# Kernel tuning notes

Measured on AMD Instinct MI355X. Metric: run time of the kernel, lower is better.

The kernel has to match this reference:

```python
import jax, jax.numpy as jnp
import numpy as np

D_MODEL = 256
D_STATE = 128          # d_model // 2
D_CONV = 4
EXPAND = 4
D_INNER = EXPAND * D_MODEL  # 1024
DT_RANK = (D_MODEL + 15) // 16  # 16
N_HEADS = 8
D_FF = 4 * D_MODEL
EPS = 1e-6


def layer_norm(x, a, b):
    # torch LayerNorm-like but with unbiased std (ddof=1) per the source
    mean = jnp.mean(x, axis=-1, keepdims=True)
    d = x.shape[-1]
    var = jnp.sum((x - mean) ** 2, axis=-1, keepdims=True) / (d - 1)
    std = jnp.sqrt(var)
    return a * (x - mean) / (std + EPS) + b


def silu(x):
    return x * jax.nn.sigmoid(x)


def mamba(x, in_proj_w, conv_w, conv_b, x_proj_w, dt_proj_w, dt_proj_b, A_log, Dp, out_proj_w):
    B, L, _ = x.shape
    xz = jnp.einsum('bld,ed->ble', x, in_proj_w)  # (B,L,2*D_INNER)
    xi, z = xz[..., :D_INNER], xz[..., D_INNER:]
    # causal depthwise conv1d over L
    xp = jnp.pad(xi, ((0, 0), (D_CONV - 1, 0), (0, 0)))
    u = conv_b
    for k in range(D_CONV):
        u = u + xp[:, k:k + L, :] * conv_w[:, k]
    u = silu(u)  # (B,L,D_INNER)
    dbl = jnp.einsum('bld,ed->ble', u, x_proj_w)  # (B,L,DT_RANK+2*D_STATE)
    dt = dbl[..., :DT_RANK]
    Bm = dbl[..., DT_RANK:DT_RANK + D_STATE]
    Cm = dbl[..., DT_RANK + D_STATE:]
    dt = jax.nn.softplus(jnp.einsum('blr,dr->bld', dt, dt_proj_w) + dt_proj_b)  # (B,L,D_INNER)
    A = -jnp.exp(A_log)  # (D_INNER, D_STATE)
    dA = jnp.exp(jnp.einsum('bld,dn->bldn', dt, A))          # (B,L,Din,N)
    dBu = jnp.einsum('bld,bln,bld->bldn', dt, Bm, u)          # (B,L,Din,N)

    def step(h, inp):
        dA_t, dBu_t, C_t = inp
        h = dA_t * h + dBu_t                    # (B,Din,N)
        y = jnp.einsum('bdn,bn->bd', h, C_t)    # (B,Din)
        return h, y

    h0 = jnp.zeros((B, D_INNER, D_STATE), dtype=x.dtype)
    _, ys = jax.lax.scan(step, h0, (jnp.swapaxes(dA, 0, 1), jnp.swapaxes(dBu, 0, 1), jnp.swapaxes(Cm, 0, 1)))
    y = jnp.swapaxes(ys, 0, 1) + u * Dp  # (B,L,Din)
    y = y * silu(z)
    return jnp.einsum('ble,de->bld', y, out_proj_w)


def cross_attention(q_in, kv_in, mask, wq_w, wq_b, wk_w, wk_b, wv_w, wv_b, wo_w, wo_b):
    B, Lq, _ = q_in.shape
    Lk = kv_in.shape[1]
    dk = D_MODEL // N_HEADS
    q = (jnp.einsum('bld,ed->ble', q_in, wq_w) + wq_b).reshape(B, Lq, N_HEADS, dk).transpose(0, 2, 1, 3)
    k = (jnp.einsum('bld,ed->ble', kv_in, wk_w) + wk_b).reshape(B, Lk, N_HEADS, dk).transpose(0, 2, 1, 3)
    v = (jnp.einsum('bld,ed->ble', kv_in, wv_w) + wv_b).reshape(B, Lk, N_HEADS, dk).transpose(0, 2, 1, 3)
    scores = jnp.einsum('bhqd,bhkd->bhqk', q, k) / np.sqrt(dk)
    # mask: (B,1,Lk) bool -> broadcast (B,1,1,Lk)
    scores = jnp.where(mask[:, None, :, :], scores, jnp.finfo(scores.dtype).min)
    p = jax.nn.softmax(scores, axis=-1)
    o = jnp.einsum('bhqk,bhkd->bhqd', p, v).transpose(0, 2, 1, 3).reshape(B, Lq, D_MODEL)
    return jnp.einsum('ble,de->bld', o, wo_w) + wo_b


def setup_inputs() -> dict:
    key = jax.random.key(0)
    ks = jax.random.split(key, 24)
    s = 0.02
    B, L, Lm = 2, 512, 512
    inp = {
        'x': jax.random.normal(ks[0], (B, L, D_MODEL), jnp.float32),
        'memory': jax.random.normal(ks[1], (B, Lm, D_MODEL), jnp.float32),
        'src_mask': jnp.ones((B, 1, Lm), bool),
        'tgt_mask': jnp.ones((B, 1, L), bool),
        # mamba params
        'in_proj_w': jax.random.normal(ks[2], (2 * D_INNER, D_MODEL)) * s,
        'conv_w': jax.random.normal(ks[3], (D_INNER, D_CONV)) * s,
        'conv_b': jnp.zeros((D_INNER,)),
        'x_proj_w': jax.random.normal(ks[4], (DT_RANK + 2 * D_STATE, D_INNER)) * s,
        'dt_proj_w': jax.random.normal(ks[5], (D_INNER, DT_RANK)) * s,
        'dt_proj_b': jnp.log(jnp.expm1(0.01)) * jnp.ones((D_INNER,)),
        'A_log': jnp.log(jnp.broadcast_to(jnp.arange(1, D_STATE + 1, dtype=jnp.float32), (D_INNER, D_STATE))),
        'Dp': jnp.ones((D_INNER,)),
        'out_proj_w': jax.random.normal(ks[6], (D_MODEL, D_INNER)) * s,
        # norms
        'norm1_a': jnp.ones((D_MODEL,)), 'norm1_b': jnp.zeros((D_MODEL,)),
        'norm2_a': jnp.ones((D_MODEL,)), 'norm2_b': jnp.zeros((D_MODEL,)),
        'norm3_a': jnp.ones((D_MODEL,)), 'norm3_b': jnp.zeros((D_MODEL,)),
        # cross attention
        'wq_w': jax.random.normal(ks[7], (D_MODEL, D_MODEL)) * s, 'wq_b': jnp.zeros((D_MODEL,)),
        'wk_w': jax.random.normal(ks[8], (D_MODEL, D_MODEL)) * s, 'wk_b': jnp.zeros((D_MODEL,)),
        'wv_w': jax.random.normal(ks[9], (D_MODEL, D_MODEL)) * s, 'wv_b': jnp.zeros((D_MODEL,)),
        'wo_w': jax.random.normal(ks[10], (D_MODEL, D_MODEL)) * s, 'wo_b': jnp.zeros((D_MODEL,)),
        # ffn
        'w1_w': jax.random.normal(ks[11], (D_FF, D_MODEL)) * s, 'w1_b': jnp.zeros((D_FF,)),
        'w2_w': jax.random.normal(ks[12], (D_MODEL, D_FF)) * s, 'w2_b': jnp.zeros((D_MODEL,)),
    }
    return inp


def reference(x, memory, src_mask, tgt_mask,
              in_proj_w, conv_w, conv_b, x_proj_w, dt_proj_w, dt_proj_b, A_log, Dp, out_proj_w,
              norm1_a, norm1_b, norm2_a, norm2_b, norm3_a, norm3_b,
              wq_w, wq_b, wk_w, wk_b, wv_w, wv_b, wo_w, wo_b,
              w1_w, w1_b, w2_w, w2_b):
    # self mamba block (pre-norm, residual); dropout = 0
    h = x + mamba(layer_norm(x, norm1_a, norm1_b), in_proj_w, conv_w, conv_b,
                  x_proj_w, dt_proj_w, dt_proj_b, A_log, Dp, out_proj_w)
    # cross attention block
    h = h + cross_attention(layer_norm(h, norm2_a, norm2_b), memory, src_mask,
                            wq_w, wq_b, wk_w, wk_b, wv_w, wv_b, wo_w, wo_b)
    # ffn block
    hn = layer_norm(h, norm3_a, norm3_b)
    ff = jnp.einsum('blf,df->bld', jax.nn.relu(jnp.einsum('bld,fd->blf', hn, w1_w) + w1_b), w2_w) + w2_b
    return h + ff
```

## Files before the change

### kernel.cpp

```cpp
#include <hip/hip_runtime.h>
#include <hip/hip_bf16.h>

#define B_SZ 2
#define L_SEQ 512
#define D_MODEL 256
#define D_STATE 128
#define D_CONV 4
#define D_INNER 1024
#define DT_RANK 16
#define N_HEADS 8
#define DK 32
#define D_FF 1024
#define R_TOT (B_SZ * L_SEQ)
#define DBL_LD (DT_RANK + 2 * D_STATE)
#define NSEG 16
#define SEGL 32
#define DPB 4

typedef __hip_bfloat16 bf16;
typedef __attribute__((ext_vector_type(8))) short short8;
typedef __attribute__((ext_vector_type(4))) float floatx4;

__device__ inline float fexp(float x) { return __expf(x); }
__device__ inline float fexp2(float x) { return __builtin_amdgcn_exp2f(x); }
__device__ inline float frcp(float x) { return __builtin_amdgcn_rcpf(x); }
__device__ inline float silu_f(float x) { return x * frcp(1.f + fexp(-x)); }
__device__ inline float softplus_f(float x) { return (x > 20.f) ? x : __logf(1.f + fexp(x)); }
__device__ inline float bf2f(unsigned short u) { return __uint_as_float(((unsigned)u) << 16); }

__device__ inline float swz_xor16(float x) {
    return __int_as_float(__builtin_amdgcn_ds_swizzle(__float_as_int(x), 0x401F));
}

#define S_MEM 262144
#define S_INW 524288
#define S_XPW 278528
#define S_OPW 262144
#define S_WQ  65536
#define S_WK  65536
#define S_WV  65536
#define S_WO  65536
#define S_W1  262144
#define S_W2  262144
#define S_TOT (S_MEM+S_INW+S_XPW+S_OPW+S_WQ+S_WK+S_WV+S_WO+S_W1+S_W2)
#define PACK_BLKS ((S_TOT + 255) / 256)
#define Z1_F4 (3 * R_TOT * D_MODEL / 4)
#define Z2_F4 (R_TOT * D_MODEL / 4)
#define Z3_F4 (R_TOT * DBL_LD / 4)
#define ZERO_BLKS ((Z1_F4 + Z2_F4 + Z3_F4 + 255) / 256)

__global__ __launch_bounds__(256) void pack_ln1(
    const float* __restrict__ s0, const float* __restrict__ s1,
    const float* __restrict__ s2, const float* __restrict__ s3,
    const float* __restrict__ s4, const float* __restrict__ s5,
    const float* __restrict__ s6, const float* __restrict__ s7,
    const float* __restrict__ s8, const float* __restrict__ s9,
    bf16* __restrict__ dst,
    const float* __restrict__ X, const float* __restrict__ a,
    const float* __restrict__ bvec, bf16* __restrict__ ln1b,
    float* __restrict__ zero1, float* __restrict__ zero2,
    float* __restrict__ zero3)
{
    __shared__ float r1[256], r2[256];
    if (blockIdx.x < PACK_BLKS) {
        const long i = (long)blockIdx.x * 256 + threadIdx.x;
        if (i >= S_TOT) return;
        const long off[11] = {0, S_MEM, S_MEM+S_INW, S_MEM+S_INW+S_XPW,
            S_MEM+S_INW+S_XPW+S_OPW, S_MEM+S_INW+S_XPW+S_OPW+S_WQ,
            S_MEM+S_INW+S_XPW+S_OPW+S_WQ+S_WK,
            S_MEM+S_INW+S_XPW+S_OPW+S_WQ+S_WK+S_WV,
            S_MEM+S_INW+S_XPW+S_OPW+S_WQ+S_WK+S_WV+S_WO,
            S_MEM+S_INW+S_XPW+S_OPW+S_WQ+S_WK+S_WV+S_WO+S_W1, S_TOT};
        const float* srcs[10] = {s0,s1,s2,s3,s4,s5,s6,s7,s8,s9};
        int seg = 0;
#pragma unroll
        for (int k = 1; k < 10; ++k) if (i >= off[k]) seg = k;
        dst[i] = __float2bfloat16(srcs[seg][i - off[seg]]);
    } else if (blockIdx.x < PACK_BLKS + R_TOT) {
        const int row = blockIdx.x - PACK_BLKS;
        const int t = threadIdx.x;
        const float v = X[(long)row * D_MODEL + t];
        r1[t] = v;
        r2[t] = v * v;
        __syncthreads();
        for (int s = 128; s > 0; s >>= 1) {
            if (t < s) { r1[t] += r1[t + s]; r2[t] += r2[t + s]; }
            __syncthreads();
        }
        const float mean = r1[0] * (1.f / 256.f);
        const float var = (r2[0] - 256.f * mean * mean) * (1.f / 255.f);
        const float sd = sqrtf(fmaxf(var, 0.f));
        const float o = a[t] * (v - mean) / (sd + 1e-6f) + bvec[t];
        ln1b[(long)row * D_MODEL + t] = __float2bfloat16(o);
    } else {
        const long i4 = (long)(blockIdx.x - PACK_BLKS - R_TOT) * 256 + threadIdx.x;
        const float4 z = {0.f, 0.f, 0.f, 0.f};
        if (i4 < Z1_F4)                      *(float4*)&zero1[i4 * 4] = z;
        else if (i4 < Z1_F4 + Z2_F4)          *(float4*)&zero2[(i4 - Z1_F4) * 4] = z;
        else if (i4 < Z1_F4 + Z2_F4 + Z3_F4)  *(float4*)&zero3[(i4 - Z1_F4 - Z2_F4) * 4] = z;
    }
}

template <int EPI>
__global__ __launch_bounds__(256) void mfma_gemm(
    const bf16* __restrict__ A, const bf16* __restrict__ W, int K,
    float* __restrict__ C, bf16* __restrict__ Cb, int ldc,
    const float* __restrict__ bias, const float* __restrict__ res,
    int M, int N)
{
    const int wave = threadIdx.x >> 6;
    const int lane = threadIdx.x & 63;
    const int row16 = lane & 15;
    const int quad  = lane >> 4;
    const int bm = blockIdx.y * 64 + wave * 16;
    const int bn = blockIdx.x * 64;

    floatx4 acc[4];
#pragma unroll
    for (int t = 0; t < 4; ++t) acc[t] = (floatx4){0.f, 0.f, 0.f, 0.f};

    const long arow = (long)(bm + row16) * K;
    for (int k0 = 0; k0 < K; k0 += 32) {
        const short8 av = *(const short8*)(A + arow + k0 + quad * 8);
#pragma unroll
        for (int t = 0; t < 4; ++t) {
            const int gn = bn + t * 16 + row16;
            short8 bv = {0,0,0,0,0,0,0,0};
            if (gn < N) bv = *(const short8*)(W + (long)gn * K + k0 + quad * 8);
            acc[t] = __builtin_amdgcn_mfma_f32_16x16x32_bf16(av, bv, acc[t], 0, 0, 0);
        }
    }

#pragma unroll
    for (int t = 0; t < 4; ++t) {
        const int gn = bn + t * 16 + row16;
        if (gn >= N) continue;
        const float bs = bias ? bias[gn] : 0.f;
#pragma unroll
        for (int r = 0; r < 4; ++r) {
            const int gm = bm + quad * 4 + r;
            float v = acc[t][r] + bs;
            if (EPI == 1) v = fmaxf(v, 0.f);
            const long ci = (long)gm * ldc + gn;
            if (res) v += res[ci];
            if (C)  C[ci] = v;
            if (Cb) Cb[ci] = __float2bfloat16(v);
        }
    }
}

template <int SK>
__global__ __launch_bounds__(256) void splitk_gemm(
    const bf16* __restrict__ A, const bf16* __restrict__ W, int K,
    float* __restrict__ C, int ldc,
    const float* __restrict__ bias, const float* __restrict__ res,
    int M, int N)
{
    const int wave = threadIdx.x >> 6;
    const int lane = threadIdx.x & 63;
    const int row16 = lane & 15;
    const int quad  = lane >> 4;
    const int bm = blockIdx.y * 64 + wave * 16;
    const int bn = blockIdx.x * 64;
    const int kz = blockIdx.z;
    const int ksl = K / SK;
    const int kbeg = kz * ksl;

    floatx4 acc[4];
#pragma unroll
    for (int t = 0; t < 4; ++t) acc[t] = (floatx4){0.f, 0.f, 0.f, 0.f};

    const long arow = (long)(bm + row16) * K;
    for (int k0 = kbeg; k0 < kbeg + ksl; k0 += 32) {
        const short8 av = *(const short8*)(A + arow + k0 + quad * 8);
#pragma unroll
        for (int t = 0; t < 4; ++t) {
            const int gn = bn + t * 16 + row16;
            short8 bv = {0,0,0,0,0,0,0,0};
            if (gn < N) bv = *(const short8*)(W + (long)gn * K + k0 + quad * 8);
            acc[t] = __builtin_amdgcn_mfma_f32_16x16x32_bf16(av, bv, acc[t], 0, 0, 0);
        }
    }

#pragma unroll
    for (int t = 0; t < 4; ++t) {
        const int gn = bn + t * 16 + row16;
        if (gn >= N) continue;
        const float bs = (kz == 0 && bias) ? bias[gn] : 0.f;
#pragma unroll
        for (int r = 0; r < 4; ++r) {
            const int gm = bm + quad * 4 + r;
            float v = acc[t][r] + bs;
            const long ci = (long)gm * ldc + gn;
            if (kz == 0 && res) v += res[ci];
            atomicAdd(&C[ci], v);
        }
    }
}

__global__ __launch_bounds__(256) void xproj_kv_gemm(
    const bf16* __restrict__ ub, const bf16* __restrict__ XPWb,
    float* __restrict__ dbl,
    const bf16* __restrict__ memb, const bf16* __restrict__ WKb,
    const bf16* __restrict__ WVb,
    const float* __restrict__ WKB, const float* __restrict__ WVB,
    float* __restrict__ kb, float* __restrict__ vb)
{
    const int wave = threadIdx.x >> 6;
    const int lane = threadIdx.x & 63;
    const int row16 = lane & 15;
    const int quad  = lane >> 4;
    const int bm = blockIdx.y * 64 + wave * 16;
    const int bn = blockIdx.x * 64;
    const int z = blockIdx.z;

    const bf16* A; const bf16* W; const float* bias; float* C;
    int K, N, ldc, kbeg, ksl;
    if (z < 4) {
        A = ub; W = XPWb; bias = nullptr; C = dbl;
        K = D_INNER; N = DBL_LD; ldc = DBL_LD;
        ksl = D_INNER / 4; kbeg = z * ksl;
    } else {
        if (bn >= D_MODEL) return;
        const int zz = z - 4;
        const int which = zz >> 1;
        const int kz = zz & 1;
        A = memb; W = which ? WVb : WKb;
        bias = (kz == 0) ? (which ? WVB : WKB) : nullptr;
        C = which ? vb : kb;
        K = D_MODEL; N = D_MODEL; ldc = D_MODEL;
        ksl = D_MODEL / 2; kbeg = kz * ksl;
    }

    floatx4 acc[4];
#pragma unroll
    for (int t = 0; t < 4; ++t) acc[t] = (floatx4){0.f, 0.f, 0.f, 0.f};

    const long arow = (long)(bm + row16) * K;
    for (int k0 = kbeg; k0 < kbeg + ksl; k0 += 32) {
        const short8 av = *(const short8*)(A + arow + k0 + quad * 8);
#pragma unroll
        for (int t = 0; t < 4; ++t) {
            const int gn = bn + t * 16 + row16;
            short8 bv = {0,0,0,0,0,0,0,0};
            if (gn < N) bv = *(const short8*)(W + (long)gn * K + k0 + quad * 8);
            acc[t] = __builtin_amdgcn_mfma_f32_16x16x32_bf16(av, bv, acc[t], 0, 0, 0);
        }
    }

#pragma unroll
    for (int t = 0; t < 4; ++t) {
        const int gn = bn + t * 16 + row16;
        if (gn >= N) continue;
        const float bs = bias ? bias[gn] : 0.f;
#pragma unroll
        for (int r = 0; r < 4; ++r) {
            const int gm = bm + quad * 4 + r;
            atomicAdd(&C[(long)gm * ldc + gn], acc[t][r] + bs);
        }
    }
}

__global__ __launch_bounds__(256) void gemm16_ln(
    const bf16* __restrict__ A, const bf16* __restrict__ W, int K,
    const float* __restrict__ bias, const float* __restrict__ res,
    float* __restrict__ Cf,
    const float* __restrict__ lna, const float* __restrict__ lnb,
    bf16* __restrict__ lnout)
{
    __shared__ float tile[16][264];
    __shared__ float red1[16][16];
    __shared__ float red2[16][16];
    const int w = threadIdx.x >> 6;
    const int lane = threadIdx.x & 63;
    const int row16 = lane & 15;
    const int quad  = lane >> 4;
    const int bm = blockIdx.x * 16;

    floatx4 acc[4];
#pragma unroll
    for (int t = 0; t < 4; ++t) acc[t] = (floatx4){0.f, 0.f, 0.f, 0.f};

    const long arow = (long)(bm + row16) * K;
    for (int k0 = 0; k0 < K; k0 += 32) {
        const short8 av = *(const short8*)(A + arow + k0 + quad * 8);
#pragma unroll
        for (int t = 0; t < 4; ++t) {
            const int gn = w * 64 + t * 16 + row16;
            const short8 bv = *(const short8*)(W + (long)gn * K + k0 + quad * 8);
            acc[t] = __builtin_amdgcn_mfma_f32_16x16x32_bf16(av, bv, acc[t], 0, 0, 0);
        }
    }

#pragma unroll
    for (int t = 0; t < 4; ++t) {
        const int gn = w * 64 + t * 16 + row16;
        const float bs = bias ? bias[gn] : 0.f;
#pragma unroll
        for (int r = 0; r < 4; ++r) {
            const int gm = bm + quad * 4 + r;
            float v = acc[t][r] + bs;
            const long ci = (long)gm * D_MODEL + gn;
            if (res) v += res[ci];
            Cf[ci] = v;
            tile[quad * 4 + r][gn] = v;
        }
    }
    __syncthreads();

    const int r = threadIdx.x >> 4;
    const int g = threadIdx.x & 15;
    float s = 0.f, q = 0.f;
#pragma unroll
    for (int i = 0; i < 16; ++i) {
        const float x = tile[r][g * 16 + i];
        s += x; q += x * x;
    }
    red1[r][g] = s; red2[r][g] = q;
    __syncthreads();
    float ts = 0.f, tq = 0.f;
#pragma unroll
    for (int i = 0; i < 16; ++i) { ts += red1[r][i]; tq += red2[r][i]; }
    const float mean = ts * (1.f / 256.f);
    const float var = (tq - 256.f * mean * mean) * (1.f / 255.f);
    const float sd = sqrtf(fmaxf(var, 0.f));
    const long rowbase = (long)(bm + r) * D_MODEL;
#pragma unroll
    for (int i = 0; i < 16; ++i) {
        const int c = g * 16 + i;
        const float o = lna[c] * (tile[r][c] - mean) / (sd + 1e-6f) + lnb[c];
        lnout[rowbase + c] = __float2bfloat16(o);
    }
}

__global__ __launch_bounds__(256) void ln_kernel(
    const float* __restrict__ x, const float* __restrict__ a,
    const float* __restrict__ bvec, bf16* __restrict__ out)
{
    const int row = blockIdx.x;
    const int t = threadIdx.x;
    const float v = x[(long)row * D_MODEL + t];
    __shared__ float r1[256], r2[256];
    r1[t] = v;
    r2[t] = v * v;
    __syncthreads();
    for (int s = 128; s > 0; s >>= 1) {
        if (t < s) { r1[t] += r1[t + s]; r2[t] += r2[t + s]; }
        __syncthreads();
    }
    const float mean = r1[0] * (1.f / 256.f);
    const float var = (r2[0] - 256.f * mean * mean) * (1.f / 255.f);
    const float sd = sqrtf(fmaxf(var, 0.f));
    const float o = a[t] * (v - mean) / (sd + 1e-6f) + bvec[t];
    out[(long)row * D_MODEL + t] = __float2bfloat16(o);
}

__global__ __launch_bounds__(256) void dt_gemm_T(
    const float* __restrict__ A , const float* __restrict__ W ,
    const float* __restrict__ bias, float* __restrict__ dtT)
{
    __shared__ float As[DT_RANK][65];
    __shared__ float Bs[DT_RANK][65];
    __shared__ float Ct[64][65];
    const int bm = blockIdx.y * 64;
    const int bn = blockIdx.x * 64;
    const int tid = threadIdx.x;
    const int tx = tid & 15;
    const int ty = tid >> 4;
    const int r = tid >> 2;
    const int kk = (tid & 3) * 4;
#pragma unroll
    for (int q = 0; q < 4; ++q) {
        As[kk + q][r] = A[(long)(bm + r) * DBL_LD + kk + q];
        Bs[kk + q][r] = W[(long)(bn + r) * DT_RANK + kk + q];
    }
    __syncthreads();
    float acc[4][4] = {};
#pragma unroll
    for (int k = 0; k < DT_RANK; ++k) {
        float a[4], bv[4];
#pragma unroll
        for (int i = 0; i < 4; ++i) a[i] = As[k][ty * 4 + i];
#pragma unroll
        for (int j = 0; j < 4; ++j) bv[j] = Bs[k][tx * 4 + j];
#pragma unroll
        for (int i = 0; i < 4; ++i)
#pragma unroll
            for (int j = 0; j < 4; ++j)
                acc[i][j] = fmaf(a[i], bv[j], acc[i][j]);
    }
#pragma unroll
    for (int i = 0; i < 4; ++i)
#pragma unroll
        for (int j = 0; j < 4; ++j)
            Ct[tx * 4 + j][ty * 4 + i] = softplus_f(acc[i][j] + bias[bn + tx * 4 + j]);
    __syncthreads();
    const int b = bm >> 9;
    const int l0 = bm & 511;
    const int r2 = tid >> 4;
    const int c4 = (tid & 15) * 4;
#pragma unroll
    for (int q = 0; q < 4; ++q) {
        const int dl = r2 + q * 16;
        float4 v = {Ct[dl][c4], Ct[dl][c4 + 1], Ct[dl][c4 + 2], Ct[dl][c4 + 3]};
        *(float4*)&dtT[((long)(b * D_INNER + bn + dl) << 9) + l0 + c4] = v;
    }
}

__global__ __launch_bounds__(256) void conv_silu_T(
    const bf16* __restrict__ xz, const float* __restrict__ cw,
    const float* __restrict__ cb, bf16* __restrict__ ub, float* __restrict__ uT)
{
    __shared__ float t[64][65];
    const int db = blockIdx.x;
    const int lb = blockIdx.y;
    const int b  = blockIdx.z;
    const int tid = threadIdx.x;
    const int r  = tid >> 4;
    const int c4 = (tid & 15) * 4;
    const int d0 = db * 64 + c4;

    const float4 cb4 = *(const float4*)&cb[d0];
    float cwa[4][4];
#pragma unroll
    for (int i = 0; i < 4; ++i) {
        const float4 w = *(const float4*)&cw[(d0 + i) * 4];
        cwa[i][0] = w.x; cwa[i][1] = w.y; cwa[i][2] = w.z; cwa[i][3] = w.w;
    }

#pragma unroll
    for (int q = 0; q < 4; ++q) {
        const int ll = r + q * 16;
        const int l = lb * 64 + ll;
        float s0 = cb4.x, s1 = cb4.y, s2 = cb4.z, s3 = cb4.w;
#pragma unroll
        for (int k = 0; k < D_CONV; ++k) {
            const int ls = l - 3 + k;
            if (ls >= 0) {
                const ushort4 xv = *(const ushort4*)&xz[((long)(b * L_SEQ + ls)) * (2 * D_INNER) + d0];
                s0 = fmaf(bf2f(xv.x), cwa[0][k], s0);
                s1 = fmaf(bf2f(xv.y), cwa[1][k], s1);
                s2 = fmaf(bf2f(xv.z), cwa[2][k], s2);
                s3 = fmaf(bf2f(xv.w), cwa[3][k], s3);
            }
        }
        s0 = silu_f(s0); s1 = silu_f(s1); s2 = silu_f(s2); s3 = silu_f(s3);
        bf16 b0 = __float2bfloat16(s0), b1 = __float2bfloat16(s1);
        bf16 b2 = __float2bfloat16(s2), b3 = __float2bfloat16(s3);
        ushort4 pk;
        pk.x = *reinterpret_cast<unsigned short*>(&b0);
        pk.y = *reinterpret_cast<unsigned short*>(&b1);
        pk.z = *reinterpret_cast<unsigned short*>(&b2);
        pk.w = *reinterpret_cast<unsigned short*>(&b3);
        *reinterpret_cast<ushort4*>(ub + ((long)(b * L_SEQ + l)) * D_INNER + d0) = pk;
        t[c4 + 0][ll] = s0; t[c4 + 1][ll] = s1;
        t[c4 + 2][ll] = s2; t[c4 + 3][ll] = s3;
    }
    __syncthreads();
#pragma unroll
    for (int q = 0; q < 4; ++q) {
        const int dl = r + q * 16;
        float4 v = {t[dl][c4], t[dl][c4 + 1], t[dl][c4 + 2], t[dl][c4 + 3]};
        *(float4*)&uT[((long)(b * D_INNER + db * 64 + dl) << 9) + lb * 64 + c4] = v;
    }
}

__global__ __launch_bounds__(1024) void scan_fused(
    const float* __restrict__ dtT, const float* __restrict__ uT,
    const float* __restrict__ dbl, const float* __restrict__ A_log,
    const float* __restrict__ Dp, const bf16* __restrict__ xz,
    bf16* __restrict__ yb)
{
    const int b  = blockIdx.x >> 8;
    const int d0 = (blockIdx.x & 255) * DPB;
    const int w = threadIdx.x >> 6;
    const int lane = threadIdx.x & 63;
    const int n0 = lane * 2;

    __shared__ float Sh[NSEG][DPB][D_STATE];
    __shared__ float Ph[NSEG][DPB][D_STATE];

    float An0[DPB], An1[DPB];
#pragma unroll
    for (int di = 0; di < DPB; ++di) {
        An0[di] = -fexp(A_log[(long)(d0 + di) * D_STATE + n0]) * 1.44269504f;
        An1[di] = -fexp(A_log[(long)(d0 + di) * D_STATE + n0 + 1]) * 1.44269504f;
    }
    const float4 dp4 = *(const float4*)&Dp[d0];
    const float dpc[4] = {dp4.x, dp4.y, dp4.z, dp4.w};

    const float* blp = dbl + ((long)(b * L_SEQ + w * SEGL)) * DBL_LD + DT_RANK + n0;
    const float* clp = blp + D_STATE;
    const long tbase = ((long)(b * D_INNER + d0) << 9) + w * SEGL;

    if (w < NSEG - 1) {
        float h0[DPB] = {}, h1[DPB] = {}, sdt[DPB] = {};
        for (int s = 0; s < SEGL / 4; ++s) {
            float2 Bv[4];
#pragma unroll
            for (int j = 0; j < 4; ++j)
                Bv[j] = *(const float2*)(blp + (long)(s * 4 + j) * DBL_LD);
#pragma unroll
            for (int di = 0; di < DPB; ++di) {
                const float4 dt0 = *(const float4*)(dtT + tbase + ((long)di << 9) + s * 4);
                const float4 u0  = *(const float4*)(uT  + tbase + ((long)di << 9) + s * 4);
                const float dts[4] = {dt0.x, dt0.y, dt0.z, dt0.w};
                const float us[4]  = {u0.x, u0.y, u0.z, u0.w};
#pragma unroll
                for (int j = 0; j < 4; ++j) {
                    const float dtv = dts[j];
                    sdt[di] += dtv;
                    const float dtu = dtv * us[j];
                    h0[di] = fmaf(fexp2(dtv * An0[di]), h0[di], dtu * Bv[j].x);
                    h1[di] = fmaf(fexp2(dtv * An1[di]), h1[di], dtu * Bv[j].y);
                }
            }
        }
#pragma unroll
        for (int di = 0; di < DPB; ++di) {
            Sh[w][di][n0]     = h0[di];
            Sh[w][di][n0 + 1] = h1[di];
            Ph[w][di][n0]     = fexp2(An0[di] * sdt[di]);
            Ph[w][di][n0 + 1] = fexp2(An1[di] * sdt[di]);
        }
    }
    __syncthreads();

    float h0[DPB] = {}, h1[DPB] = {};
    for (int s = 0; s < w; ++s) {
#pragma unroll
        for (int di = 0; di < DPB; ++di) {
            h0[di] = fmaf(Ph[s][di][n0],     h0[di], Sh[s][di][n0]);
            h1[di] = fmaf(Ph[s][di][n0 + 1], h1[di], Sh[s][di][n0 + 1]);
        }
    }

    const int bpa = (lane ^ 32) << 2;
    const bool lo32 = lane < 32;
    const bool b16 = (lane & 16) != 0;
    const int g = lane >> 4;
    const bool wl = (lane & 15) == 15;

    for (int s = 0; s < SEGL / 4; ++s) {
        float2 Bv[4], Cv[4];
#pragma unroll
        for (int j = 0; j < 4; ++j) {
            Bv[j] = *(const float2*)(blp + (long)(s * 4 + j) * DBL_LD);
            Cv[j] = *(const float2*)(clp + (long)(s * 4 + j) * DBL_LD);
        }
        float zsel[DPB];
#pragma unroll
        for (int di = 0; di < DPB; ++di) {
            const float4 dt0 = *(const float4*)(dtT + tbase + ((long)di << 9) + s * 4);
            const float4 u0  = *(const float4*)(uT  + tbase + ((long)di << 9) + s * 4);
            const float dts[4] = {dt0.x, dt0.y, dt0.z, dt0.w};
            const float us[4]  = {u0.x, u0.y, u0.z, u0.w};
            float yp[4];
#pragma unroll
            for (int j = 0; j < 4; ++j) {
                const float dtv = dts[j];
                const float dtu = dtv * us[j];
                h0[di] = fmaf(fexp2(dtv * An0[di]), h0[di], dtu * Bv[j].x);
                h1[di] = fmaf(fexp2(dtv * An1[di]), h1[di], dtu * Bv[j].y);
                yp[j] = fmaf(h0[di], Cv[j].x, h1[di] * Cv[j].y);
            }
            if (lane == 0) {
#pragma unroll
                for (int j = 0; j < 4; ++j)
                    yp[j] = fmaf(us[j], dpc[di], yp[j]);
            }
            float z0[2];
#pragma unroll
            for (int j = 0; j < 2; ++j) {
                const float t = lo32 ? yp[j]     : yp[j + 2];
                const float u = lo32 ? yp[j + 2] : yp[j];
                z0[j] = t + __int_as_float(
                    __builtin_amdgcn_ds_bpermute(bpa, __float_as_int(u)));
            }
            float z2;
            {
                const float t = b16 ? z0[1] : z0[0];
                const float u = b16 ? z0[0] : z0[1];
                z2 = t + swz_xor16(u);
            }
            z2 += __int_as_float(__builtin_amdgcn_update_dpp(0, __float_as_int(z2), 0x111, 0xf, 0xf, true));
            z2 += __int_as_float(__builtin_amdgcn_update_dpp(0, __float_as_int(z2), 0x112, 0xf, 0xf, true));
            z2 += __int_as_float(__builtin_amdgcn_update_dpp(0, __float_as_int(z2), 0x114, 0xf, 0xf, true));
            z2 += __int_as_float(__builtin_amdgcn_update_dpp(0, __float_as_int(z2), 0x118, 0xf, 0xf, true));
            zsel[di] = z2;
        }
        if (wl) {
            const int l = w * SEGL + s * 4 + g;
            const long row = (long)b * L_SEQ + l;
            const ushort4 zu = *(const ushort4*)&xz[row * (2 * D_INNER) + D_INNER + d0];
            const float y0 = zsel[0] * silu_f(bf2f(zu.x));
            const float y1 = zsel[1] * silu_f(bf2f(zu.y));
            const float y2 = zsel[2] * silu_f(bf2f(zu.z));
            const float y3 = zsel[3] * silu_f(bf2f(zu.w));
            bf16 o0 = __float2bfloat16(y0), o1 = __float2bfloat16(y1);
            bf16 o2 = __float2bfloat16(y2), o3 = __float2bfloat16(y3);
            ushort4 pk;
            pk.x = *reinterpret_cast<unsigned short*>(&o0);
            pk.y = *reinterpret_cast<unsigned short*>(&o1);
            pk.z = *reinterpret_cast<unsigned short*>(&o2);
            pk.w = *reinterpret_cast<unsigned short*>(&o3);
            *reinterpret_cast<ushort4*>(yb + row * D_INNER + d0) = pk;
        }
    }
}

#define QT 16
#define CK 64

__global__ __launch_bounds__(256) void attn_kernel(
    const bf16* __restrict__ ln2b, const bf16* __restrict__ WQb,
    const float* __restrict__ WQB,
    const float* __restrict__ k, const float* __restrict__ v,
    bf16* __restrict__ o)
{
    const int qt = blockIdx.x;
    const int hh = blockIdx.y;
    const int b  = blockIdx.z;
    const int t = threadIdx.x;

    __shared__ float qs[QT][33];
    __shared__ float Ks[CK][36];
    __shared__ float Vs[CK][36];

    {
        const int qr = t >> 4;
        const int c  = (t * 2) & 31;
        const bf16* ar = ln2b + ((long)(b * L_SEQ + qt * QT + qr)) * D_MODEL;
        const bf16* w0 = WQb + (long)(hh * DK + c) * D_MODEL;
        const bf16* w1 = w0 + D_MODEL;
        float a0 = 0.f, a1 = 0.f;
        for (int kk = 0; kk < D_MODEL; kk += 4) {
            const ushort4 av = *(const ushort4*)(ar + kk);
            const ushort4 b0 = *(const ushort4*)(w0 + kk);
            const ushort4 b1 = *(const ushort4*)(w1 + kk);
            a0 = fmaf(bf2f(av.x), bf2f(b0.x), a0);
            a0 = fmaf(bf2f(av.y), bf2f(b0.y), a0);
            a0 = fmaf(bf2f(av.z), bf2f(b0.z), a0);
            a0 = fmaf(bf2f(av.w), bf2f(b0.w), a0);
            a1 = fmaf(bf2f(av.x), bf2f(b1.x), a1);
            a1 = fmaf(bf2f(av.y), bf2f(b1.y), a1);
            a1 = fmaf(bf2f(av.z), bf2f(b1.z), a1);
            a1 = fmaf(bf2f(av.w), bf2f(b1.w), a1);
        }
        qs[qr][c]     = a0 + WQB[hh * DK + c];
        qs[qr][c + 1] = a1 + WQB[hh * DK + c + 1];
    }
    __syncthreads();

    const int lane = t & 15;
    const int qa = t >> 4;
    const int q0 = qt * QT + qa;
    const float scale = 0.17677669529663687f;
    float qr0[32];
#pragma unroll
    for (int i = 0; i < 32; ++i) qr0[i] = qs[qa][i] * scale;

    float m0 = -1e30f, l0 = 0.f, o0[32] = {};

    for (int c = 0; c < L_SEQ; c += CK) {
        __syncthreads();
        {
            const int fid = t * 2;
            const int row = fid >> 3;
            const int c0  = (fid & 7) * 4;
            const float* kp = k + ((long)(b * L_SEQ + c + row) * D_MODEL + hh * DK + c0);
            const float* vp = v + ((long)(b * L_SEQ + c + row) * D_MODEL + hh * DK + c0);
            *(float4*)&Ks[row][c0]     = *(const float4*)kp;
            *(float4*)&Ks[row][c0 + 4] = *(const float4*)(kp + 4);
            *(float4*)&Vs[row][c0]     = *(const float4*)vp;
            *(float4*)&Vs[row][c0 + 4] = *(const float4*)(vp + 4);
        }
        __syncthreads();

        float s0[4];
#pragma unroll
        for (int i = 0; i < 4; ++i) {
            const int kk = i * 16 + lane;
            float a0 = 0.f;
#pragma unroll
            for (int dd = 0; dd < 32; dd += 4) {
                const float4 kv = *(const float4*)&Ks[kk][dd];
                a0 = fmaf(qr0[dd+0], kv.x, a0); a0 = fmaf(qr0[dd+1], kv.y, a0);
                a0 = fmaf(qr0[dd+2], kv.z, a0); a0 = fmaf(qr0[dd+3], kv.w, a0);
            }
            s0[i] = a0;
        }

        float cm0 = s0[0];
#pragma unroll
        for (int i = 1; i < 4; ++i) cm0 = fmaxf(cm0, s0[i]);
#pragma unroll
        for (int off = 8; off > 0; off >>= 1)
            cm0 = fmaxf(cm0, __shfl_down(cm0, off, 16));
        cm0 = __shfl(cm0, 0, 16);

        const float nm0 = fmaxf(m0, cm0);
        const float al0 = fexp(m0 - nm0);
        l0 *= al0;
#pragma unroll
        for (int dd = 0; dd < 32; ++dd) o0[dd] *= al0;
        m0 = nm0;

        float p0[4];
#pragma unroll
        for (int i = 0; i < 4; ++i) { p0[i] = fexp(s0[i] - m0); l0 += p0[i]; }

#pragma unroll
        for (int i = 0; i < 4; ++i) {
            const int kk = i * 16 + lane;
#pragma unroll
            for (int dd = 0; dd < 32; dd += 4) {
                const float4 vv = *(const float4*)&Vs[kk][dd];
                o0[dd+0] = fmaf(p0[i], vv.x, o0[dd+0]);
                o0[dd+1] = fmaf(p0[i], vv.y, o0[dd+1]);
                o0[dd+2] = fmaf(p0[i], vv.z, o0[dd+2]);
                o0[dd+3] = fmaf(p0[i], vv.w, o0[dd+3]);
            }
        }
    }

#pragma unroll
    for (int off = 8; off > 0; off >>= 1) {
        l0 += __shfl_down(l0, off, 16);
#pragma unroll
        for (int dd = 0; dd < 32; ++dd) o0[dd] += __shfl_down(o0[dd], off, 16);
    }
    if (lane == 0) {
        const float i0 = 1.f / l0;
        bf16* op0 = o + ((long)(b * L_SEQ + q0) * D_MODEL + hh * DK);
#pragma unroll
        for (int dd = 0; dd < 32; ++dd) op0[dd] = __float2bfloat16(o0[dd] * i0);
    }
}


extern "C" void kernel_launch(void* const* d_in, const int* in_sizes, int n_in,
                              void* d_out, int out_size, void* d_ws, size_t ws_size,
                              hipStream_t stream) {
    const float* X   = (const float*)d_in[0];
    const float* MEM = (const float*)d_in[1];
    const float* CW  = (const float*)d_in[5];
    const float* CB  = (const float*)d_in[6];
    const float* DTW = (const float*)d_in[8];
    const float* DTB = (const float*)d_in[9];
    const float* ALG = (const float*)d_in[10];
    const float* DP  = (const float*)d_in[11];
    const float* N1A = (const float*)d_in[13];
    const float* N1B = (const float*)d_in[14];
    const float* N2A = (const float*)d_in[15];
    const float* N2B = (const float*)d_in[16];
    const float* N3A = (const float*)d_in[17];
    const float* N3B = (const float*)d_in[18];
    const float* WQB = (const float*)d_in[20];
    const float* WKB = (const float*)d_in[22];
    const float* WVB = (const float*)d_in[24];
    const float* WOB = (const float*)d_in[26];
    const float* W1B = (const float*)d_in[28];
    const float* W2B = (const float*)d_in[30];
    const float* INW = (const float*)d_in[4];
    const float* XPW = (const float*)d_in[7];
    const float* OPW = (const float*)d_in[12];
    const float* WQ  = (const float*)d_in[19];
    const float* WKw = (const float*)d_in[21];
    const float* WVw = (const float*)d_in[23];
    const float* WO  = (const float*)d_in[25];
    const float* W1  = (const float*)d_in[27];
    const float* W2  = (const float*)d_in[29];
    float* out = (float*)d_out;

    bf16* bp = (bf16*)d_ws;
    bf16* ub   = bp;  bp += (long)R_TOT * D_INNER;
    bf16* ybb  = bp;  bp += (long)R_TOT * D_INNER;
    bf16* ffab = ybb;
    bf16* xzb  = bp;  bp += (long)R_TOT * 2 * D_INNER;
    bf16* ln1b = bp;  bp += (long)R_TOT * D_MODEL;
    bf16* aob  = ln1b;
    bf16* ln2b = bp;  bp += (long)R_TOT * D_MODEL;
    bf16* ln3b = ln2b;
    bf16* arena = bp; bp += S_TOT;
    bf16* MEMb = arena;
    bf16* INWb = MEMb + S_MEM;
    bf16* XPWb = INWb + S_INW;
    bf16* OPWb = XPWb + S_XPW;
    bf16* WQb  = OPWb + S_OPW;
    bf16* WKb  = WQb + S_WQ;
    bf16* WVb  = WKb + S_WK;
    bf16* WOb  = WVb + S_WV;
    bf16* W1b  = WOb + S_WO;
    bf16* W2b  = W1b + S_W1;

    float* p = (float*)(bp + ((((long)(bp - (bf16*)d_ws)) & 1) ? 1 : 0));
    float* uT  = p;                                  p += (long)R_TOT * D_INNER;
    float* dbl = p;                                  p += (long)R_TOT * DBL_LD;
    float* dtT = p;                                  p += (long)R_TOT * D_INNER;
    float* kb  = p;                                  p += (long)R_TOT * D_MODEL;
    float* vb  = p;                                  p += (long)R_TOT * D_MODEL;
    float* h1  = p;                                  p += (long)R_TOT * D_MODEL;
    float* h2  = p;                                  p += (long)R_TOT * D_MODEL;

    const dim3 blk256(256);
    const int MT64 = R_TOT / 64;

    pack_ln1<<<PACK_BLKS + R_TOT + ZERO_BLKS, blk256, 0, stream>>>(
        MEM, INW, XPW, OPW, WQ, WKw, WVw, WO, W1, W2, arena,
        X, N1A, N1B, ln1b, kb, out, dbl);

    mfma_gemm<0><<<dim3(2 * D_INNER / 64, MT64), blk256, 0, stream>>>(
        ln1b, INWb, D_MODEL, nullptr, xzb, 2 * D_INNER, nullptr, nullptr,
        R_TOT, 2 * D_INNER);

    conv_silu_T<<<dim3(D_INNER / 64, L_SEQ / 64, B_SZ), blk256, 0, stream>>>(
        xzb, CW, CB, ub, uT);

    xproj_kv_gemm<<<dim3((DBL_LD + 63) / 64, MT64, 8), blk256, 0, stream>>>(
        ub, XPWb, dbl, MEMb, WKb, WVb, WKB, WVB, kb, vb);

    dt_gemm_T<<<dim3(D_INNER / 64, MT64), blk256, 0, stream>>>(dbl, DTW, DTB, dtT);

    scan_fused<<<B_SZ * D_INNER / DPB, dim3(1024), 0, stream>>>(
        dtT, uT, dbl, ALG, DP, xzb, ybb);

    splitk_gemm<4><<<dim3(D_MODEL / 64, MT64, 4), blk256, 0, stream>>>(
        ybb, OPWb, D_INNER, h1, D_MODEL, nullptr, X, R_TOT, D_MODEL);

    ln_kernel<<<R_TOT, blk256, 0, stream>>>(h1, N2A, N2B, ln2b);

    attn_kernel<<<dim3(L_SEQ / QT, N_HEADS, B_SZ), blk256, 0, stream>>>(
        ln2b, WQb, WQB, kb, vb, aob);

    gemm16_ln<<<R_TOT / 16, blk256, 0, stream>>>(
        aob, WOb, D_MODEL, WOB, h1, h2, N3A, N3B, ln3b);

    mfma_gemm<1><<<dim3(D_FF / 64, MT64), blk256, 0, stream>>>(
        ln3b, W1b, D_MODEL, nullptr, ffab, D_FF, W1B, nullptr, R_TOT, D_FF);

    splitk_gemm<4><<<dim3(D_MODEL / 64, MT64, 4), blk256, 0, stream>>>(
        ffab, W2b, D_FF, out, D_MODEL, W2B, h2, R_TOT, D_MODEL);

    (void)in_sizes; (void)n_in; (void)out_size; (void)ws_size;
}
```

Baseline: 332.7 us.

## Vectorize weight packing, store K/V as bf16 without split-K atomics, wave-per-row LayerNorm

The weight-pack stage now converts four floats per thread with float4 loads and packed bf16 stores. The K/V projection no longer splits K across blocks and accumulates with float atomics; it writes bf16 K/V directly, which removes two zeroed buffers and halves attention's K/V load bytes. The LayerNorm kernel uses one wave per row with shuffle reductions instead of a shared-memory tree, and the Q projection in attention uses 8-wide loads. K/V are rounded to bf16, which slightly lowers precision.

```diff
diff --git a/kernel.cpp b/kernel.cpp
--- a/kernel.cpp
+++ b/kernel.cpp
@@ -43,8 +43,8 @@
 #define S_W1  262144
 #define S_W2  262144
 #define S_TOT (S_MEM+S_INW+S_XPW+S_OPW+S_WQ+S_WK+S_WV+S_WO+S_W1+S_W2)
-#define PACK_BLKS ((S_TOT + 255) / 256)
-#define Z1_F4 (3 * R_TOT * D_MODEL / 4)
+#define PACK_BLKS (S_TOT / 4 / 256)
+#define Z1_F4 (R_TOT * D_MODEL / 4)
 #define Z2_F4 (R_TOT * D_MODEL / 4)
 #define Z3_F4 (R_TOT * DBL_LD / 4)
 #define ZERO_BLKS ((Z1_F4 + Z2_F4 + Z3_F4 + 255) / 256)
@@ -63,8 +63,7 @@
 {
     __shared__ float r1[256], r2[256];
     if (blockIdx.x < PACK_BLKS) {
-        const long i = (long)blockIdx.x * 256 + threadIdx.x;
-        if (i >= S_TOT) return;
+        const long e0 = ((long)blockIdx.x * 256 + threadIdx.x) * 4;
         const long off[11] = {0, S_MEM, S_MEM+S_INW, S_MEM+S_INW+S_XPW,
             S_MEM+S_INW+S_XPW+S_OPW, S_MEM+S_INW+S_XPW+S_OPW+S_WQ,
             S_MEM+S_INW+S_XPW+S_OPW+S_WQ+S_WK,
@@ -74,8 +73,16 @@
         const float* srcs[10] = {s0,s1,s2,s3,s4,s5,s6,s7,s8,s9};
         int seg = 0;
 #pragma unroll
-        for (int k = 1; k < 10; ++k) if (i >= off[k]) seg = k;
-        dst[i] = __float2bfloat16(srcs[seg][i - off[seg]]);
+        for (int k = 1; k < 10; ++k) if (e0 >= off[k]) seg = k;
+        const float4 v = *(const float4*)&srcs[seg][e0 - off[seg]];
+        bf16 b0 = __float2bfloat16(v.x), b1 = __float2bfloat16(v.y);
+        bf16 b2 = __float2bfloat16(v.z), b3 = __float2bfloat16(v.w);
+        ushort4 pk;
+        pk.x = *reinterpret_cast<unsigned short*>(&b0);
+        pk.y = *reinterpret_cast<unsigned short*>(&b1);
+        pk.z = *reinterpret_cast<unsigned short*>(&b2);
+        pk.w = *reinterpret_cast<unsigned short*>(&b3);
+        *reinterpret_cast<ushort4*>(dst + e0) = pk;
     } else if (blockIdx.x < PACK_BLKS + R_TOT) {
         const int row = blockIdx.x - PACK_BLKS;
         const int t = threadIdx.x;
@@ -204,7 +211,7 @@
     const bf16* __restrict__ memb, const bf16* __restrict__ WKb,
     const bf16* __restrict__ WVb,
     const float* __restrict__ WKB, const float* __restrict__ WVB,
-    float* __restrict__ kb, float* __restrict__ vb)
+    bf16* __restrict__ kbb, bf16* __restrict__ vbb)
 {
     const int wave = threadIdx.x >> 6;
     const int lane = threadIdx.x & 63;
@@ -214,49 +221,59 @@
     const int bn = blockIdx.x * 64;
     const int z = blockIdx.z;
 
-    const bf16* A; const bf16* W; const float* bias; float* C;
-    int K, N, ldc, kbeg, ksl;
+    floatx4 acc[4];
+#pragma unroll
+    for (int t = 0; t < 4; ++t) acc[t] = (floatx4){0.f, 0.f, 0.f, 0.f};
+
     if (z < 4) {
-        A = ub; W = XPWb; bias = nullptr; C = dbl;
-        K = D_INNER; N = DBL_LD; ldc = DBL_LD;
-        ksl = D_INNER / 4; kbeg = z * ksl;
+        const int K = D_INNER, N = DBL_LD;
+        const int ksl = D_INNER / 4, kbeg = z * ksl;
+        const long arow = (long)(bm + row16) * K;
+        for (int k0 = kbeg; k0 < kbeg + ksl; k0 += 32) {
+            const short8 av = *(const short8*)(ub + arow + k0 + quad * 8);
+#pragma unroll
+            for (int t = 0; t < 4; ++t) {
+                const int gn = bn + t * 16 + row16;
+                short8 bv = {0,0,0,0,0,0,0,0};
+                if (gn < N) bv = *(const short8*)(XPWb + (long)gn * K + k0 + quad * 8);
+                acc[t] = __builtin_amdgcn_mfma_f32_16x16x32_bf16(av, bv, acc[t], 0, 0, 0);
+            }
+        }
+#pragma unroll
+        for (int t = 0; t < 4; ++t) {
+            const int gn = bn + t * 16 + row16;
+            if (gn >= N) continue;
+#pragma unroll
+            for (int r = 0; r < 4; ++r) {
+                const int gm = bm + quad * 4 + r;
+                atomicAdd(&dbl[(long)gm * DBL_LD + gn], acc[t][r]);
+            }
+        }
     } else {
         if (bn >= D_MODEL) return;
-        const int zz = z - 4;
-        const int which = zz >> 1;
-        const int kz = zz & 1;
-        A = memb; W = which ? WVb : WKb;
-        bias = (kz == 0) ? (which ? WVB : WKB) : nullptr;
-        C = which ? vb : kb;
-        K = D_MODEL; N = D_MODEL; ldc = D_MODEL;
-        ksl = D_MODEL / 2; kbeg = kz * ksl;
-    }
-
-    floatx4 acc[4];
-#pragma unroll
-    for (int t = 0; t < 4; ++t) acc[t] = (floatx4){0.f, 0.f, 0.f, 0.f};
-
-    const long arow = (long)(bm + row16) * K;
-    for (int k0 = kbeg; k0 < kbeg + ksl; k0 += 32) {
-        const short8 av = *(const short8*)(A + arow + k0 + quad * 8);
+        const int which = z - 4;
+        const bf16* W = which ? WVb : WKb;
+        const float* bias = which ? WVB : WKB;
+        bf16* O = which ? vbb : kbb;
+        const long arow = (long)(bm + row16) * D_MODEL;
+        for (int k0 = 0; k0 < D_MODEL; k0 += 32) {
+            const short8 av = *(const short8*)(memb + arow + k0 + quad * 8);
+#pragma unroll
+            for (int t = 0; t < 4; ++t) {
+                const int gn = bn + t * 16 + row16;
+                const short8 bv = *(const short8*)(W + (long)gn * D_MODEL + k0 + quad * 8);
+                acc[t] = __builtin_amdgcn_mfma_f32_16x16x32_bf16(av, bv, acc[t], 0, 0, 0);
+            }
+        }
 #pragma unroll
         for (int t = 0; t < 4; ++t) {
             const int gn = bn + t * 16 + row16;
-            short8 bv = {0,0,0,0,0,0,0,0};
-            if (gn < N) bv = *(const short8*)(W + (long)gn * K + k0 + quad * 8);
-            acc[t] = __builtin_amdgcn_mfma_f32_16x16x32_bf16(av, bv, acc[t], 0, 0, 0);
-        }
-    }
-
-#pragma unroll
-    for (int t = 0; t < 4; ++t) {
-        const int gn = bn + t * 16 + row16;
-        if (gn >= N) continue;
-        const float bs = bias ? bias[gn] : 0.f;
-#pragma unroll
-        for (int r = 0; r < 4; ++r) {
-            const int gm = bm + quad * 4 + r;
-            atomicAdd(&C[(long)gm * ldc + gn], acc[t][r] + bs);
+            const float bs = bias[gn];
+#pragma unroll
+            for (int r = 0; r < 4; ++r) {
+                const int gm = bm + quad * 4 + r;
+                O[(long)gm * D_MODEL + gn] = __float2bfloat16(acc[t][r] + bs);
+            }
         }
     }
 }
@@ -337,22 +354,33 @@
     const float* __restrict__ x, const float* __restrict__ a,
     const float* __restrict__ bvec, bf16* __restrict__ out)
 {
-    const int row = blockIdx.x;
-    const int t = threadIdx.x;
-    const float v = x[(long)row * D_MODEL + t];
-    __shared__ float r1[256], r2[256];
-    r1[t] = v;
-    r2[t] = v * v;
-    __syncthreads();
-    for (int s = 128; s > 0; s >>= 1) {
-        if (t < s) { r1[t] += r1[t + s]; r2[t] += r2[t + s]; }
-        __syncthreads();
-    }
-    const float mean = r1[0] * (1.f / 256.f);
-    const float var = (r2[0] - 256.f * mean * mean) * (1.f / 255.f);
+    const int row = blockIdx.x * 4 + (threadIdx.x >> 6);
+    const int lane = threadIdx.x & 63;
+    const float4 v = *(const float4*)&x[((long)row << 8) + lane * 4];
+    float s = v.x + v.y + v.z + v.w;
+    float q = fmaf(v.x, v.x, fmaf(v.y, v.y, fmaf(v.z, v.z, v.w * v.w)));
+#pragma unroll
+    for (int off = 32; off > 0; off >>= 1) {
+        s += __shfl_xor(s, off, 64);
+        q += __shfl_xor(q, off, 64);
+    }
+    const float mean = s * (1.f / 256.f);
+    const float var = (q - 256.f * mean * mean) * (1.f / 255.f);
     const float sd = sqrtf(fmaxf(var, 0.f));
-    const float o = a[t] * (v - mean) / (sd + 1e-6f) + bvec[t];
-    out[(long)row * D_MODEL + t] = __float2bfloat16(o);
+    const float4 a4 = *(const float4*)&a[lane * 4];
+    const float4 b4 = *(const float4*)&bvec[lane * 4];
+    const float o0 = a4.x * (v.x - mean) / (sd + 1e-6f) + b4.x;
+    const float o1 = a4.y * (v.y - mean) / (sd + 1e-6f) + b4.y;
+    const float o2 = a4.z * (v.z - mean) / (sd + 1e-6f) + b4.z;
+    const float o3 = a4.w * (v.w - mean) / (sd + 1e-6f) + b4.w;
+    bf16 c0 = __float2bfloat16(o0), c1 = __float2bfloat16(o1);
+    bf16 c2 = __float2bfloat16(o2), c3 = __float2bfloat16(o3);
+    ushort4 pk;
+    pk.x = *reinterpret_cast<unsigned short*>(&c0);
+    pk.y = *reinterpret_cast<unsigned short*>(&c1);
+    pk.z = *reinterpret_cast<unsigned short*>(&c2);
+    pk.w = *reinterpret_cast<unsigned short*>(&c3);
+    *reinterpret_cast<ushort4*>(out + ((long)row << 8) + lane * 4) = pk;
 }
 
 __global__ __launch_bounds__(256) void dt_gemm_T(
@@ -615,7 +643,7 @@
 __global__ __launch_bounds__(256) void attn_kernel(
     const bf16* __restrict__ ln2b, const bf16* __restrict__ WQb,
     const float* __restrict__ WQB,
-    const float* __restrict__ k, const float* __restrict__ v,
+    const bf16* __restrict__ kbb, const bf16* __restrict__ vbb,
     bf16* __restrict__ o)
 {
     const int qt = blockIdx.x;
@@ -634,18 +662,16 @@
         const bf16* w0 = WQb + (long)(hh * DK + c) * D_MODEL;
         const bf16* w1 = w0 + D_MODEL;
         float a0 = 0.f, a1 = 0.f;
-        for (int kk = 0; kk < D_MODEL; kk += 4) {
-            const ushort4 av = *(const ushort4*)(ar + kk);
-            const ushort4 b0 = *(const ushort4*)(w0 + kk);
-            const ushort4 b1 = *(const ushort4*)(w1 + kk);
-            a0 = fmaf(bf2f(av.x), bf2f(b0.x), a0);
-            a0 = fmaf(bf2f(av.y), bf2f(b0.y), a0);
-            a0 = fmaf(bf2f(av.z), bf2f(b0.z), a0);
-            a0 = fmaf(bf2f(av.w), bf2f(b0.w), a0);
-            a1 = fmaf(bf2f(av.x), bf2f(b1.x), a1);
-            a1 = fmaf(bf2f(av.y), bf2f(b1.y), a1);
-            a1 = fmaf(bf2f(av.z), bf2f(b1.z), a1);
-            a1 = fmaf(bf2f(av.w), bf2f(b1.w), a1);
+        for (int kk = 0; kk < D_MODEL; kk += 8) {
+            const short8 av = *(const short8*)(ar + kk);
+            const short8 b0 = *(const short8*)(w0 + kk);
+            const short8 b1 = *(const short8*)(w1 + kk);
+#pragma unroll
+            for (int e = 0; e < 8; ++e) {
+                const float af = bf2f((unsigned short)av[e]);
+                a0 = fmaf(af, bf2f((unsigned short)b0[e]), a0);
+                a1 = fmaf(af, bf2f((unsigned short)b1[e]), a1);
+            }
         }
         qs[qr][c]     = a0 + WQB[hh * DK + c];
         qs[qr][c + 1] = a1 + WQB[hh * DK + c + 1];
@@ -665,15 +691,24 @@
     for (int c = 0; c < L_SEQ; c += CK) {
         __syncthreads();
         {
-            const int fid = t * 2;
-            const int row = fid >> 3;
-            const int c0  = (fid & 7) * 4;
-            const float* kp = k + ((long)(b * L_SEQ + c + row) * D_MODEL + hh * DK + c0);
-            const float* vp = v + ((long)(b * L_SEQ + c + row) * D_MODEL + hh * DK + c0);
-            *(float4*)&Ks[row][c0]     = *(const float4*)kp;
-            *(float4*)&Ks[row][c0 + 4] = *(const float4*)(kp + 4);
-            *(float4*)&Vs[row][c0]     = *(const float4*)vp;
-            *(float4*)&Vs[row][c0 + 4] = *(const float4*)(vp + 4);
+            const int row = t >> 2;
+            const int c0  = (t & 3) * 8;
+            const long base = (long)(b * L_SEQ + c + row) * D_MODEL + hh * DK + c0;
+            const short8 k8 = *(const short8*)(kbb + base);
+            const short8 v8 = *(const short8*)(vbb + base);
+            float4 f;
+            f.x = bf2f((unsigned short)k8[0]); f.y = bf2f((unsigned short)k8[1]);
+            f.z = bf2f((unsigned short)k8[2]); f.w = bf2f((unsigned short)k8[3]);
+            *(float4*)&Ks[row][c0] = f;
+            f.x = bf2f((unsigned short)k8[4]); f.y = bf2f((unsigned short)k8[5]);
+            f.z = bf2f((unsigned short)k8[6]); f.w = bf2f((unsigned short)k8[7]);
+            *(float4*)&Ks[row][c0 + 4] = f;
+            f.x = bf2f((unsigned short)v8[0]); f.y = bf2f((unsigned short)v8[1]);
+            f.z = bf2f((unsigned short)v8[2]); f.w = bf2f((unsigned short)v8[3]);
+            *(float4*)&Vs[row][c0] = f;
+            f.x = bf2f((unsigned short)v8[4]); f.y = bf2f((unsigned short)v8[5]);
+            f.z = bf2f((unsigned short)v8[6]); f.w = bf2f((unsigned short)v8[7]);
+            *(float4*)&Vs[row][c0 + 4] = f;
         }
         __syncthreads();
 
@@ -782,6 +817,8 @@
     bf16* aob  = ln1b;
     bf16* ln2b = bp;  bp += (long)R_TOT * D_MODEL;
     bf16* ln3b = ln2b;
+    bf16* kbb  = bp;  bp += (long)R_TOT * D_MODEL;
+    bf16* vbb  = bp;  bp += (long)R_TOT * D_MODEL;
     bf16* arena = bp; bp += S_TOT;
     bf16* MEMb = arena;
     bf16* INWb = MEMb + S_MEM;
@@ -798,8 +835,6 @@
     float* uT  = p;                                  p += (long)R_TOT * D_INNER;
     float* dbl = p;                                  p += (long)R_TOT * DBL_LD;
     float* dtT = p;                                  p += (long)R_TOT * D_INNER;
-    float* kb  = p;                                  p += (long)R_TOT * D_MODEL;
-    float* vb  = p;                                  p += (long)R_TOT * D_MODEL;
     float* h1  = p;                                  p += (long)R_TOT * D_MODEL;
     float* h2  = p;                                  p += (long)R_TOT * D_MODEL;
 
@@ -808,7 +843,7 @@
 
     pack_ln1<<<PACK_BLKS + R_TOT + ZERO_BLKS, blk256, 0, stream>>>(
         MEM, INW, XPW, OPW, WQ, WKw, WVw, WO, W1, W2, arena,
-        X, N1A, N1B, ln1b, kb, out, dbl);
+        X, N1A, N1B, ln1b, h1, out, dbl);
 
     mfma_gemm<0><<<dim3(2 * D_INNER / 64, MT64), blk256, 0, stream>>>(
         ln1b, INWb, D_MODEL, nullptr, xzb, 2 * D_INNER, nullptr, nullptr,
@@ -817,8 +852,8 @@
     conv_silu_T<<<dim3(D_INNER / 64, L_SEQ / 64, B_SZ), blk256, 0, stream>>>(
         xzb, CW, CB, ub, uT);
 
-    xproj_kv_gemm<<<dim3((DBL_LD + 63) / 64, MT64, 8), blk256, 0, stream>>>(
-        ub, XPWb, dbl, MEMb, WKb, WVb, WKB, WVB, kb, vb);
+    xproj_kv_gemm<<<dim3((DBL_LD + 63) / 64, MT64, 6), blk256, 0, stream>>>(
+        ub, XPWb, dbl, MEMb, WKb, WVb, WKB, WVB, kbb, vbb);
 
     dt_gemm_T<<<dim3(D_INNER / 64, MT64), blk256, 0, stream>>>(dbl, DTW, DTB, dtT);
 
@@ -828,10 +863,10 @@
     splitk_gemm<4><<<dim3(D_MODEL / 64, MT64, 4), blk256, 0, stream>>>(
         ybb, OPWb, D_INNER, h1, D_MODEL, nullptr, X, R_TOT, D_MODEL);
 
-    ln_kernel<<<R_TOT, blk256, 0, stream>>>(h1, N2A, N2B, ln2b);
+    ln_kernel<<<R_TOT / 4, blk256, 0, stream>>>(h1, N2A, N2B, ln2b);
 
     attn_kernel<<<dim3(L_SEQ / QT, N_HEADS, B_SZ), blk256, 0, stream>>>(
-        ln2b, WQb, WQB, kb, vb, aob);
+        ln2b, WQb, WQB, kbb, vbb, aob);
 
     gemm16_ln<<<R_TOT / 16, blk256, 0, stream>>>(
         aob, WOb, D_MODEL, WOB, h1, h2, N3A, N3B, ln3b);
```

Result: no change. 327.2 us (-1.6%).
